# Kernel tuning notes

Measured on AMD Instinct MI355X. Metric: run time of the kernel, lower is better.

## Reference

```python
import jax, jax.numpy as jnp
import numpy as np

R = 1  # local_window_radius (kernel = 2R+1 = 3)


def setup_inputs() -> dict:
    key = jax.random.key(0)
    ks = jax.random.split(key, 4)
    b, c, h, w, v = 4, 128, 96, 192, 2
    scale = 1.0 / np.sqrt(c).astype(np.float32)
    return {
        "feature0": jax.random.normal(ks[0], (b, c, h, w), jnp.float32),
        "flow": jax.random.normal(ks[1], (b, v, h, w), jnp.float32),
        "Wq": jax.random.normal(ks[2], (c, c), jnp.float32) * scale,
        "bq": jnp.zeros((c,), jnp.float32),
        "Wk": jax.random.normal(ks[3], (c, c), jnp.float32) * scale,
        "bk": jnp.zeros((c,), jnp.float32),
    }


def _windows(x, r):
    # x: [b, C, h, w] -> [b, h, w, C, k^2], zero-padded 3x3 neighborhoods.
    # Window element order matches F.unfold: row-major over (dy, dx).
    b, C, h, w = x.shape
    xp = jnp.pad(x, ((0, 0), (0, 0), (r, r), (r, r)))
    k = 2 * r + 1
    wins = [xp[:, :, dy:dy + h, dx:dx + w] for dy in range(k) for dx in range(k)]
    return jnp.stack(wins, axis=-1).transpose(0, 2, 3, 1, 4)


def reference(feature0, flow, Wq, bq, Wk, bk):
    b, c, h, w = feature0.shape
    f = feature0.transpose(0, 2, 3, 1)              # [b,h,w,c]
    q = f @ Wq.T + bq                                # q_proj -> [b,h,w,c]
    kproj = (f @ Wk.T + bk).transpose(0, 3, 1, 2)    # k_proj -> [b,c,h,w]
    k_win = _windows(kproj, R)                       # [b,h,w,c,k2]
    v_win = _windows(flow, R)                        # [b,h,w,v,k2]
    scores = jnp.einsum('bhwc,bhwck->bhwk', q, k_win) / jnp.sqrt(jnp.asarray(c, q.dtype))
    prob = jax.nn.softmax(scores, axis=-1)           # [b,h,w,k2]
    out = jnp.einsum('bhwk,bhwvk->bhwv', prob, v_win)
    return out.transpose(0, 3, 1, 2)                 # [b,v,h,w]
```

## Files before the change

kernel.cpp:

```cpp
#include <hip/hip_runtime.h>
#include <hip/hip_bf16.h>
#include <math.h>

#define B_   4
#define C_   128
#define H_   96
#define W_   192
#define HW_  (H_*W_)

#define TH 4
#define TW 16
#define HX 18
#define HPX 108
#define SHS 136

typedef __attribute__((ext_vector_type(8))) short bf16x8;
typedef __attribute__((ext_vector_type(4))) float f32x4;

__device__ __forceinline__ unsigned f2bfu(float f) {
    __hip_bfloat16 h = __float2bfloat16(f);
    return (unsigned)*(unsigned short*)&h;
}
__device__ __forceinline__ float bflo(unsigned u) { return __uint_as_float(u << 16); }
__device__ __forceinline__ float bfhi(unsigned u) { return __uint_as_float(u & 0xFFFF0000u); }

__device__ __forceinline__ bf16x8 pack8(const float* v) {
    int4 q;
    q.x = (int)(f2bfu(v[0]) | (f2bfu(v[1]) << 16));
    q.y = (int)(f2bfu(v[2]) | (f2bfu(v[3]) << 16));
    q.z = (int)(f2bfu(v[4]) | (f2bfu(v[5]) << 16));
    q.w = (int)(f2bfu(v[6]) | (f2bfu(v[7]) << 16));
    return *(bf16x8*)&q;
}

__global__ __launch_bounds__(256) void prep_kernel(
    const float* __restrict__ Wq, const float* __restrict__ Wk,
    const float* __restrict__ bq, const float* __restrict__ bk,
    short* __restrict__ Apack, float* __restrict__ u2,
    float* __restrict__ v2, float* __restrict__ c0)
{
    if (blockIdx.x < 8) {
        const int rb   = blockIdx.x;
        const int t    = threadIdx.x;
        const int lane = t & 63;
        const int r    = lane & 15;
        const int row  = (rb >> 1) * 32 + (r >> 2) * 8 + (rb & 1) * 4 + (r & 3);
        const int colb = (t >> 6) * 32 + (lane >> 4) * 8;
        float a[8];
#pragma unroll
        for (int j = 0; j < 8; ++j) a[j] = 0.f;
#pragma unroll 1
        for (int c = 0; c < C_; c += 8) {
            float  wk[8];
            float4 w0[8], w1[8];
#pragma unroll
            for (int u = 0; u < 8; ++u) {
                wk[u] = Wk[(c + u) * C_ + row];
                w0[u] = *(const float4*)(Wq + (c + u) * C_ + colb);
                w1[u] = *(const float4*)(Wq + (c + u) * C_ + colb + 4);
            }
#pragma unroll
            for (int u = 0; u < 8; ++u) {
                a[0] = fmaf(wk[u], w0[u].x, a[0]); a[1] = fmaf(wk[u], w0[u].y, a[1]);
                a[2] = fmaf(wk[u], w0[u].z, a[2]); a[3] = fmaf(wk[u], w0[u].w, a[3]);
                a[4] = fmaf(wk[u], w1[u].x, a[4]); a[5] = fmaf(wk[u], w1[u].y, a[5]);
                a[6] = fmaf(wk[u], w1[u].z, a[6]); a[7] = fmaf(wk[u], w1[u].w, a[7]);
            }
        }
        bf16x8 v = pack8(a);
        *(bf16x8*)(Apack + ((size_t)rb * 256 + t) * 8) = v;
    } else {
        const int t = threadIdx.x;
        if (t < 128) {
            float a = 0.f;
            for (int c = 0; c < C_; ++c) a = fmaf(Wk[c * C_ + t], bq[c], a);
            u2[t] = a;
        } else {
            const int i = t - 128;
            float a = 0.f;
            for (int c = 0; c < C_; ++c) a = fmaf(Wq[c * C_ + i], bk[c], a);
            v2[i] = a;
        }
        if (t == 0) {
            float a = 0.f;
            for (int c = 0; c < C_; ++c) a = fmaf(bq[c], bk[c], a);
            c0[0] = a;
        }
    }
}

__global__ __launch_bounds__(256, 2) void fused_kernel(
    const float* __restrict__ f, const short* __restrict__ Apack,
    const float* __restrict__ u2v, const float* __restrict__ v2v,
    const float* __restrict__ c0p, const float* __restrict__ flow,
    float* __restrict__ out)
{
    __shared__ unsigned short sH[HPX * SHS];
    __shared__ float sS[TH][TW][9];

    const int t    = threadIdx.x;
    const int lane = t & 63;
    const int w    = t >> 6;
    const int g    = lane >> 4, p = lane & 15;

    const int wg  = blockIdx.x;
    const int idx = (wg & 7) * 144 + (wg >> 3);
    const int b   = idx / 288;
    const int rem = idx - b * 288;
    const int ty  = rem / 12, tx = rem - ty * 12;
    const int y0  = ty * TH, x0 = tx * TW;
    const float* fb = f + (size_t)b * C_ * HW_;

    float stg[7][8];
    bool  okv[7];
#pragma unroll
    for (int it = 0; it < 7; ++it) {
        int gi = it * 256 + t; if (gi > HPX * 16 - 1) gi = HPX * 16 - 1;
        const int c8 = gi / HPX;
        const int px = gi - c8 * HPX;
        const int hy = px / HX;
        const int hx = px - hy * HX;
        const int gy = y0 + hy - 1, gx = x0 + hx - 1;
        const bool ok = (gy >= 0) && (gy < H_) && (gx >= 0) && (gx < W_);
        okv[it] = ok;
        const int gyc = ok ? gy : 0, gxc = ok ? gx : 0;
        const float* src = fb + (size_t)(c8 * 8) * HW_ + gyc * W_ + gxc;
#pragma unroll
        for (int j = 0; j < 8; ++j) stg[it][j] = src[(size_t)j * HW_];
    }
#pragma unroll
    for (int it = 0; it < 7; ++it) {
        const int gi = it * 256 + t;
        if (gi < HPX * 16) {
            const int c8 = gi / HPX;
            const int px = gi - c8 * HPX;
            float v[8];
#pragma unroll
            for (int j = 0; j < 8; ++j) v[j] = okv[it] ? stg[it][j] : 0.f;
            *(bf16x8*)(sH + px * SHS + c8 * 8) = pack8(v);
        }
    }

    const int xl = lane & 15;
    const int gy = y0 + w, gx = x0 + xl;
    const int vch = g >> 1;
    float mk[9], flw9[9];
#pragma unroll
    for (int n = 0; n < 9; ++n) {
        const int yn = gy + n / 3 - 1, xn = gx + n % 3 - 1;
        const bool ok = (yn >= 0) && (yn < H_) && (xn >= 0) && (xn < W_);
        mk[n] = ok ? 1.f : 0.f;
        const int spn = ok ? yn * W_ + xn : gy * W_ + gx;
        flw9[n] = flow[((size_t)b * 2 + vch) * HW_ + spn];
    }
    __syncthreads();

    f32x4 acc[8];
#pragma unroll
    for (int rb = 0; rb < 8; ++rb) acc[rb] = (f32x4){0.f, 0.f, 0.f, 0.f};
#pragma unroll
    for (int ks = 0; ks < 4; ++ks) {
        const int hpx = (w + 1) * HX + (p + 1);
        const bf16x8 bfr = *(const bf16x8*)(sH + hpx * SHS + (ks * 4 + g) * 8);
#pragma unroll
        for (int rb = 0; rb < 8; ++rb) {
            const bf16x8 afr = *(const bf16x8*)(Apack +
                ((size_t)((rb * 4 + ks) * 64 + lane)) * 8);
            acc[rb] = __builtin_amdgcn_mfma_f32_16x16x32_bf16(afr, bfr, acc[rb], 0, 0, 0);
        }
    }

    uint2 pk[8];
#pragma unroll
    for (int rb = 0; rb < 8; ++rb) {
        const f32x4 uu = *(const f32x4*)(u2v + (rb >> 1) * 32 + g * 8 + (rb & 1) * 4);
        const f32x4 vv = acc[rb] + uu;
        pk[rb].x = f2bfu(vv[0]) | (f2bfu(vv[1]) << 16);
        pk[rb].y = f2bfu(vv[2]) | (f2bfu(vv[3]) << 16);
    }
    bf16x8 aS[4];
#pragma unroll
    for (int ks = 0; ks < 4; ++ks) {
        const int4 qv = make_int4((int)pk[2 * ks].x, (int)pk[2 * ks].y,
                                  (int)pk[2 * ks + 1].x, (int)pk[2 * ks + 1].y);
        aS[ks] = *(bf16x8*)&qv;
    }

#pragma unroll
    for (int dy = 0; dy < 3; ++dy) {
        const int hyy = w + dy;
        f32x4 s0 = (f32x4){0.f, 0.f, 0.f, 0.f};
        f32x4 s1 = (f32x4){0.f, 0.f, 0.f, 0.f};
#pragma unroll
        for (int ks = 0; ks < 4; ++ks) {
            const int hpx0 = hyy * HX + p;
            const bf16x8 b0 = *(const bf16x8*)(sH + hpx0 * SHS + (ks * 4 + g) * 8);
            const bf16x8 b1 = *(const bf16x8*)(sH + (hpx0 + 2) * SHS + (ks * 4 + g) * 8);
            s0 = __builtin_amdgcn_mfma_f32_16x16x32_bf16(aS[ks], b0, s0, 0, 0, 0);
            s1 = __builtin_amdgcn_mfma_f32_16x16x32_bf16(aS[ks], b1, s1, 0, 0, 0);
        }
#pragma unroll
        for (int i = 0; i < 4; ++i) {
            const int x = g * 4 + i;
            const float val = (g < 2) ? s0[i] : s1[i];
            const int   d   = (g < 2) ? (p - x) : (x - p);
            const int   n9  = (g < 2) ? (dy * 3 + d) : (dy * 3 + 2 - d);
            if ((unsigned)d <= 2u) sS[w][x][n9] = val;
        }
    }

    float beta = 0.f;
    const bool edge = (gx == 0) | (gx == W_ - 1) | (gy == 0) | (gy == H_ - 1);
    if (edge) {
        const int hpx = (w + 1) * HX + (xl + 1);
#pragma unroll
        for (int c8 = 0; c8 < 16; ++c8) {
            const uint4 hv = *(const uint4*)(sH + hpx * SHS + c8 * 8);
            const float4 va = *(const float4*)(v2v + c8 * 8);
            const float4 vb = *(const float4*)(v2v + c8 * 8 + 4);
            beta += bflo(hv.x) * va.x + bfhi(hv.x) * va.y
                  + bflo(hv.y) * va.z + bfhi(hv.y) * va.w
                  + bflo(hv.z) * vb.x + bfhi(hv.z) * vb.y
                  + bflo(hv.w) * vb.z + bfhi(hv.w) * vb.w;
        }
        beta += *c0p;
    }

    const float scale = 0.08838834764831845f;
    float sv[9], e[9];
    float m = -1e30f;
#pragma unroll
    for (int n = 0; n < 9; ++n) {
        sv[n] = (mk[n] != 0.f) ? (sS[w][xl][n] + beta) * scale : 0.f;
        m = fmaxf(m, sv[n]);
    }
    float sum = 0.f;
#pragma unroll
    for (int n = 0; n < 9; ++n) { e[n] = __expf(sv[n] - m); sum += e[n]; }
    const float inv = 1.f / sum;

    if ((g & 1) == 0) {
        float o = 0.f;
#pragma unroll
        for (int n = 0; n < 9; ++n) o += e[n] * mk[n] * flw9[n];
        out[((size_t)b * 2 + vch) * HW_ + gy * W_ + gx] = o * inv;
    }
}

extern "C" void kernel_launch(void* const* d_in, const int* in_sizes, int n_in,
                              void* d_out, int out_size, void* d_ws, size_t ws_size,
                              hipStream_t stream) {
    const float* f   = (const float*)d_in[0];
    const float* flw = (const float*)d_in[1];
    const float* Wq  = (const float*)d_in[2];
    const float* bq  = (const float*)d_in[3];
    const float* Wk  = (const float*)d_in[4];
    const float* bk  = (const float*)d_in[5];
    float* out = (float*)d_out;

    short* Apack = (short*)d_ws;
    float* u2    = (float*)(Apack + 128 * 128);
    float* v2    = u2 + 128;
    float* c0    = v2 + 128;

    prep_kernel<<<9, 256, 0, stream>>>(Wq, Wk, bq, bk, Apack, u2, v2, c0);
    fused_kernel<<<1152, 256, 0, stream>>>(f, Apack, u2, v2, c0, flw, out);
}
```

Measured before the change: 40.61 us.

## Drop register staging of feature loads and defer flow loads to raise occupancy

The halo loader no longer holds all 7x8 loaded values in registers before packing to LDS. Each iteration now loads, packs and stores directly, and skips global loads for out-of-bounds pixels. Flow neighbour loads move from before the barrier to the output stage, and launch bounds go from 2 to 4 blocks per SM. The aim is to cut register pressure so more waves stay resident. The cost is less memory-level parallelism within each thread, and flow loads now sit exposed on the tail path.

```diff
diff --git a/kernel.cpp b/kernel.cpp
--- a/kernel.cpp
+++ b/kernel.cpp
@@ -89,7 +89,7 @@
     }
 }
 
-__global__ __launch_bounds__(256, 2) void fused_kernel(
+__global__ __launch_bounds__(256, 4) void fused_kernel(
     const float* __restrict__ f, const short* __restrict__ Apack,
     const float* __restrict__ u2v, const float* __restrict__ v2v,
     const float* __restrict__ c0p, const float* __restrict__ flow,
@@ -111,47 +111,25 @@
     const int y0  = ty * TH, x0 = tx * TW;
     const float* fb = f + (size_t)b * C_ * HW_;
 
-    float stg[7][8];
-    bool  okv[7];
-#pragma unroll
-    for (int it = 0; it < 7; ++it) {
-        int gi = it * 256 + t; if (gi > HPX * 16 - 1) gi = HPX * 16 - 1;
-        const int c8 = gi / HPX;
-        const int px = gi - c8 * HPX;
-        const int hy = px / HX;
-        const int hx = px - hy * HX;
-        const int gy = y0 + hy - 1, gx = x0 + hx - 1;
-        const bool ok = (gy >= 0) && (gy < H_) && (gx >= 0) && (gx < W_);
-        okv[it] = ok;
-        const int gyc = ok ? gy : 0, gxc = ok ? gx : 0;
-        const float* src = fb + (size_t)(c8 * 8) * HW_ + gyc * W_ + gxc;
-#pragma unroll
-        for (int j = 0; j < 8; ++j) stg[it][j] = src[(size_t)j * HW_];
-    }
 #pragma unroll
     for (int it = 0; it < 7; ++it) {
         const int gi = it * 256 + t;
         if (gi < HPX * 16) {
             const int c8 = gi / HPX;
             const int px = gi - c8 * HPX;
+            const int hy = px / HX;
+            const int hx = px - hy * HX;
+            const int gy = y0 + hy - 1, gx = x0 + hx - 1;
             float v[8];
 #pragma unroll
-            for (int j = 0; j < 8; ++j) v[j] = okv[it] ? stg[it][j] : 0.f;
+            for (int j = 0; j < 8; ++j) v[j] = 0.f;
+            if ((gy >= 0) && (gy < H_) && (gx >= 0) && (gx < W_)) {
+                const float* src = fb + gy * W_ + gx;
+#pragma unroll
+                for (int j = 0; j < 8; ++j) v[j] = src[(size_t)(c8 * 8 + j) * HW_];
+            }
             *(bf16x8*)(sH + px * SHS + c8 * 8) = pack8(v);
         }
-    }
-
-    const int xl = lane & 15;
-    const int gy = y0 + w, gx = x0 + xl;
-    const int vch = g >> 1;
-    float mk[9], flw9[9];
-#pragma unroll
-    for (int n = 0; n < 9; ++n) {
-        const int yn = gy + n / 3 - 1, xn = gx + n % 3 - 1;
-        const bool ok = (yn >= 0) && (yn < H_) && (xn >= 0) && (xn < W_);
-        mk[n] = ok ? 1.f : 0.f;
-        const int spn = ok ? yn * W_ + xn : gy * W_ + gx;
-        flw9[n] = flow[((size_t)b * 2 + vch) * HW_ + spn];
     }
     __syncthreads();
 
@@ -208,6 +186,11 @@
             if ((unsigned)d <= 2u) sS[w][x][n9] = val;
         }
     }
+
+    const int r  = (lane >> 4) & 1;
+    const int v  = lane >> 5;
+    const int xl = lane & 15;
+    const int gy = y0 + w, gx = x0 + xl;
 
     float beta = 0.f;
     const bool edge = (gx == 0) | (gx == W_ - 1) | (gy == 0) | (gy == H_ - 1);
@@ -227,23 +210,29 @@
     }
 
     const float scale = 0.08838834764831845f;
-    float sv[9], e[9];
+    float sv[9], mk[9];
+    int spn[9];
     float m = -1e30f;
 #pragma unroll
     for (int n = 0; n < 9; ++n) {
-        sv[n] = (mk[n] != 0.f) ? (sS[w][xl][n] + beta) * scale : 0.f;
+        const int yn = gy + n / 3 - 1, xn = gx + n % 3 - 1;
+        const bool ok = (yn >= 0) && (yn < H_) && (xn >= 0) && (xn < W_);
+        mk[n]  = ok ? 1.f : 0.f;
+        spn[n] = ok ? yn * W_ + xn : gy * W_ + gx;
+        sv[n]  = ok ? (sS[w][xl][n] + beta) * scale : 0.f;
         m = fmaxf(m, sv[n]);
     }
-    float sum = 0.f;
+    float e[9], sum = 0.f;
 #pragma unroll
     for (int n = 0; n < 9; ++n) { e[n] = __expf(sv[n] - m); sum += e[n]; }
     const float inv = 1.f / sum;
 
-    if ((g & 1) == 0) {
+    if (r == 0) {
+        const float* f0 = flow + ((size_t)b * 2 + v) * HW_;
         float o = 0.f;
 #pragma unroll
-        for (int n = 0; n < 9; ++n) o += e[n] * mk[n] * flw9[n];
-        out[((size_t)b * 2 + vch) * HW_ + gy * W_ + gx] = o * inv;
+        for (int n = 0; n < 9; ++n) o += e[n] * mk[n] * f0[spn[n]];
+        out[((size_t)b * 2 + v) * HW_ + gy * W_ + gx] = o * inv;
     }
 }
 
```

Result: faster. 38.88 us (-4.3%).
